# Kernel optimization log

Hardware: AMD Instinct MI355X
Metric: run time of the kernel (lower is better)

Reference implementation:

```python
import jax, jax.numpy as jnp
import numpy as np

N_NODES = 20000
IN_CH = 512
HEADS = 8
CH = 64  # hidden_layer per head
E = 320000
E_LABEL = 100000


def setup_inputs() -> dict:
    key = jax.random.key(0)
    ks = jax.random.split(key, 8)
    x = jax.random.normal(ks[0], (N_NODES, IN_CH), dtype=jnp.float32)
    edge_index = jax.random.randint(ks[1], (2, E), 0, N_NODES)
    edge_label_index = jax.random.randint(ks[2], (2, E_LABEL), 0, N_NODES)
    # GATv2Conv params (share_weights=False, bias=True)
    sc = 1.0 / np.sqrt(IN_CH)
    W_l = jax.random.normal(ks[3], (IN_CH, HEADS * CH), dtype=jnp.float32) * sc
    W_r = jax.random.normal(ks[4], (IN_CH, HEADS * CH), dtype=jnp.float32) * sc
    att = jax.random.normal(ks[5], (HEADS, CH), dtype=jnp.float32) * (1.0 / np.sqrt(CH))
    bias = jnp.zeros((HEADS * CH,), dtype=jnp.float32)
    gamma = jnp.ones((HEADS * CH,), dtype=jnp.float32)
    beta = jnp.zeros((HEADS * CH,), dtype=jnp.float32)
    return {"x": x, "edge_index": edge_index, "edge_label_index": edge_label_index,
            "W_l": W_l, "W_r": W_r, "att": att, "bias": bias,
            "gamma": gamma, "beta": beta}


def reference(x, edge_index, edge_label_index, W_l, W_r, att, bias, gamma, beta):
    N = x.shape[0]
    H, C = att.shape
    src, dst = edge_index[0], edge_index[1]
    # GATv2Conv: separate source/target linear maps
    xl = (x @ W_l).reshape(N, H, C)
    xr = (x @ W_r).reshape(N, H, C)
    # per-edge attention logits (GATv2: leaky_relu BEFORE attention vector)
    e = jax.nn.leaky_relu(xl[src] + xr[dst], negative_slope=0.2)  # [E,H,C]
    alpha = jnp.einsum('ehc,hc->eh', e, att)                      # [E,H]
    # softmax over incoming edges of each destination node
    amax = jax.ops.segment_max(alpha, dst, num_segments=N)        # [N,H]
    alpha = jnp.exp(alpha - amax[dst])
    denom = jax.ops.segment_sum(alpha, dst, num_segments=N)       # [N,H]
    alpha = alpha / (denom[dst] + 1e-16)
    # scatter-add aggregation of attended source messages
    out = jax.ops.segment_sum(alpha[:, :, None] * xl[src], dst, num_segments=N)  # [N,H,C]
    out = out.reshape(N, H * C) + bias
    # BatchNorm1d (training-mode batch stats, eps=1e-5)
    mu = out.mean(axis=0)
    var = out.var(axis=0)
    out = (out - mu) * jax.lax.rsqrt(var + 1e-5) * gamma + beta
    out = jax.nn.relu(out)  # dropout is identity in deterministic reference
    # gather + dot-product link scoring
    s = out[edge_label_index[0]]
    t = out[edge_label_index[1]]
    return jnp.sum(s * t, axis=1)  # [E_LABEL]
```

## Files before the change

kernel.cpp:

```cpp
#include <hip/hip_runtime.h>
#include <hip/hip_bf16.h>
#include <cstdint>

#define IN_CH 512
#define HC    512
#define HEADS 8
#define NPACK 1024

typedef __attribute__((ext_vector_type(8))) short bf16x8;
typedef __attribute__((ext_vector_type(8))) ushort u16x8;
typedef __attribute__((ext_vector_type(4))) float f32x4;
typedef const __attribute__((address_space(1))) uint8_t* gaddr_t;
typedef __attribute__((address_space(3))) uint8_t* laddr_t;

__device__ inline ushort f2bf(float f) {
  uint32_t u = __float_as_uint(f);
  return (ushort)((u + 0x7fffu + ((u >> 16) & 1u)) >> 16);
}
__device__ inline float bf2f(ushort u) {
  return __uint_as_float(((uint32_t)u) << 16);
}

__global__ void prep(const float* __restrict__ x, ushort* __restrict__ xb,
                     const float* __restrict__ Wl, const float* __restrict__ Wr,
                     ushort* __restrict__ bt,
                     const int* __restrict__ ei, int* __restrict__ counts,
                     const int* __restrict__ eli, int* __restrict__ counts2,
                     int n4, int E, int EL, int nbc, int nbp, int nbh) {
  const int b = blockIdx.x;
  if (b < nbc) {
    const int i = b * 256 + threadIdx.x;
    if (i < n4) {
      const float4 v = ((const float4*)x)[i];
      ushort4 o;
      o.x = f2bf(v.x); o.y = f2bf(v.y); o.z = f2bf(v.z); o.w = f2bf(v.w);
      ((ushort4*)xb)[i] = o;
    }
  } else if (b < nbc + nbp) {
    const int i = (b - nbc) * 256 + threadIdx.x;
    if (i < NPACK * IN_CH) {
      const int n = i >> 9, k = i & 511;
      const float v = (n < HC) ? Wl[(size_t)k * HC + n] : Wr[(size_t)k * HC + (n - HC)];
      bt[i] = f2bf(v);
    }
  } else if (b < nbc + nbp + nbh) {
    const int e = (b - nbc - nbp) * 256 + threadIdx.x;
    if (e < E) atomicAdd(&counts[ei[E + e]], 1);
  } else {
    const int e = (b - nbc - nbp - nbh) * 256 + threadIdx.x;
    if (e < EL) atomicAdd(&counts2[eli[e]], 1);
  }
}

__global__ __launch_bounds__(256) void gemm_mfma(
    const ushort* __restrict__ xb, const ushort* __restrict__ bt,
    ushort* __restrict__ xlb, float* __restrict__ xr, int M) {
  __shared__ __align__(16) ushort As[128 * 32];
  __shared__ __align__(16) ushort Bs[128 * 32];
  const int wave = threadIdx.x >> 6, lane = threadIdx.x & 63;
  const int row0 = blockIdx.y * 128, col0 = blockIdx.x * 128;
  const int quad = lane >> 4, m16 = lane & 15;
  const int wrow = (wave >> 1) * 64, wcol = (wave & 1) * 64;
  const int srow = lane >> 2;
  const int scol = (lane & 3) * 8;
  const f32x4 zero = {0.f, 0.f, 0.f, 0.f};
  f32x4 acc[4][4];
  #pragma unroll
  for (int i = 0; i < 4; ++i)
    #pragma unroll
    for (int j = 0; j < 4; ++j) acc[i][j] = zero;

  for (int k0 = 0; k0 < IN_CH; k0 += 32) {
    #pragma unroll
    for (int c = 0; c < 2; ++c) {
      const int chunk = wave * 2 + c;
      const ushort* ga = xb + (size_t)(row0 + chunk * 16 + srow) * IN_CH + k0 + scol;
      __builtin_amdgcn_global_load_lds((gaddr_t)ga, (laddr_t)(As + chunk * 512), 16, 0, 0);
      const ushort* gb = bt + (size_t)(col0 + chunk * 16 + srow) * IN_CH + k0 + scol;
      __builtin_amdgcn_global_load_lds((gaddr_t)gb, (laddr_t)(Bs + chunk * 512), 16, 0, 0);
    }
    __syncthreads();
    bf16x8 af[4], bfr[4];
    #pragma unroll
    for (int i = 0; i < 4; ++i)
      af[i] = *(const bf16x8*)(As + (wrow + i * 16 + m16) * 32 + quad * 8);
    #pragma unroll
    for (int j = 0; j < 4; ++j)
      bfr[j] = *(const bf16x8*)(Bs + (wcol + j * 16 + m16) * 32 + quad * 8);
    #pragma unroll
    for (int i = 0; i < 4; ++i)
      #pragma unroll
      for (int j = 0; j < 4; ++j)
        acc[i][j] = __builtin_amdgcn_mfma_f32_16x16x32_bf16(af[i], bfr[j], acc[i][j], 0, 0, 0);
    __syncthreads();
  }
  const bool isL = (col0 < HC);
  #pragma unroll
  for (int i = 0; i < 4; ++i) {
    const int r = row0 + wrow + i * 16 + quad * 4;
    #pragma unroll
    for (int j = 0; j < 4; ++j) {
      const int cg = col0 + wcol + j * 16 + m16;
      #pragma unroll
      for (int t = 0; t < 4; ++t) {
        const int rr = r + t;
        if (rr < M) {
          if (isL) xlb[(size_t)rr * HC + cg] = f2bf(acc[i][j][t]);
          else     xr[(size_t)rr * HC + (cg - HC)] = acc[i][j][t];
        }
      }
    }
  }
}

__global__ void scan1(const int* __restrict__ cA, int* __restrict__ oA, int* __restrict__ bA,
                      const int* __restrict__ cB, int* __restrict__ oB, int* __restrict__ bB,
                      int Nn, int nb) {
  const int half = (blockIdx.x >= nb) ? 1 : 0;
  const int blk  = blockIdx.x - half * nb;
  const int* counts = half ? cB : cA;
  int* offsets = half ? oB : oA;
  int* bsums   = half ? bB : bA;
  __shared__ int tmp[256];
  const int t = threadIdx.x;
  const int i = blk * 256 + t;
  const int v = (i < Nn) ? counts[i] : 0;
  tmp[t] = v;
  __syncthreads();
  for (int d = 1; d < 256; d <<= 1) {
    int add = (t >= d) ? tmp[t - d] : 0;
    __syncthreads();
    tmp[t] += add;
    __syncthreads();
  }
  if (i < Nn) offsets[i] = tmp[t] - v;
  if (t == 255) bsums[blk] = tmp[255];
}

__global__ void scan2(int* __restrict__ bA, int* __restrict__ bB, int nb) {
  int* bsums = blockIdx.x ? bB : bA;
  __shared__ int tmp[256];
  const int t = threadIdx.x;
  if (t < nb) tmp[t] = bsums[t];
  __syncthreads();
  if (t == 0) {
    int run = 0;
    for (int b = 0; b < nb; ++b) { int c = tmp[b]; tmp[b] = run; run += c; }
  }
  __syncthreads();
  if (t < nb) bsums[t] = tmp[t];
}

__global__ void scan3(int* __restrict__ oA, const int* __restrict__ bA, int* __restrict__ curA,
                      int* __restrict__ oB, const int* __restrict__ bB, int* __restrict__ curB,
                      int Nn, int nb) {
  const int half = (blockIdx.x >= nb) ? 1 : 0;
  const int blk  = blockIdx.x - half * nb;
  int* offsets = half ? oB : oA;
  const int* bsums = half ? bB : bA;
  int* cursor  = half ? curB : curA;
  const int i = blk * 256 + threadIdx.x;
  if (i < Nn) {
    const int o = offsets[i] + bsums[i >> 8];
    offsets[i] = o;
    cursor[i] = o;
  }
}

__global__ void csr_fill(const int* __restrict__ ei, int* __restrict__ cursor,
                         int* __restrict__ csr_src,
                         const int* __restrict__ eli, int* __restrict__ cursor2,
                         int* __restrict__ csr_t, int* __restrict__ csr_eid,
                         int E, int EL, int nbE) {
  const int b = blockIdx.x;
  if (b < nbE) {
    const int e = b * 256 + threadIdx.x;
    if (e < E) {
      const int pos = atomicAdd(&cursor[ei[E + e]], 1);
      csr_src[pos] = ei[e];
    }
  } else {
    const int e = (b - nbE) * 256 + threadIdx.x;
    if (e < EL) {
      const int pos = atomicAdd(&cursor2[eli[e]], 1);
      csr_t[pos] = eli[EL + e];
      csr_eid[pos] = e;
    }
  }
}

__global__ __launch_bounds__(256) void gatv2_agg(
    const ushort* __restrict__ xlb, const float* xr, const float* __restrict__ att,
    const int* __restrict__ offsets, const int* __restrict__ counts,
    const int* __restrict__ csr_src, float* agg, int Nn) {
  const int node = blockIdx.x * 4 + (threadIdx.x >> 6);
  const int lane = threadIdx.x & 63;
  if (node >= Nn) return;
  const int start = offsets[node];
  const int deg   = counts[node];
  float rv[8], tv[8];
  {
    const float4* pr = (const float4*)(xr + (size_t)node * HC + lane * 8);
    const float4 r0 = pr[0], r1 = pr[1];
    rv[0]=r0.x; rv[1]=r0.y; rv[2]=r0.z; rv[3]=r0.w;
    rv[4]=r1.x; rv[5]=r1.y; rv[6]=r1.z; rv[7]=r1.w;
    const float4* pa = (const float4*)(att + lane * 8);
    const float4 t0 = pa[0], t1 = pa[1];
    tv[0]=t0.x; tv[1]=t0.y; tv[2]=t0.z; tv[3]=t0.w;
    tv[4]=t1.x; tv[5]=t1.y; tv[6]=t1.z; tv[7]=t1.w;
  }
  float acc[8] = {};
  float densum = 0.f;
  const int* ps = csr_src + start;
  auto row = [&](int idx) {
    return *(const u16x8*)(xlb + (size_t)ps[idx] * HC + lane * 8);
  };
  auto body = [&](const u16x8 cur) {
    float a[8];
    #pragma unroll
    for (int c = 0; c < 8; ++c) a[c] = bf2f((ushort)cur[c]);
    float s = 0.f;
    #pragma unroll
    for (int c = 0; c < 8; ++c) {
      const float v = a[c] + rv[c];
      s += fmaxf(v, 0.2f * v) * tv[c];
    }
    s += __shfl_xor(s, 1, 8);
    s += __shfl_xor(s, 2, 8);
    s += __shfl_xor(s, 4, 8);
    const float ea = __expf(s);
    densum += ea;
    #pragma unroll
    for (int c = 0; c < 8; ++c) acc[c] += ea * a[c];
  };

  u16x8 v0 = {}, v1 = {};
  if (deg > 0) v0 = row(0);
  if (deg > 1) v1 = row(1);
  int i = 0;
  for (; i + 2 <= deg; i += 2) {
    const u16x8 c0 = v0;
    if (i + 2 < deg) v0 = row(i + 2);
    body(c0);
    const u16x8 c1 = v1;
    if (i + 3 < deg) v1 = row(i + 3);
    body(c1);
  }
  if (i < deg) body(v0);

  const float inv = 1.0f / (densum + 1e-16f);
  float* pd = agg + (size_t)node * HC + lane * 8;
  *(float4*)(pd + 0) = make_float4(acc[0] * inv, acc[1] * inv, acc[2] * inv, acc[3] * inv);
  *(float4*)(pd + 4) = make_float4(acc[4] * inv, acc[5] * inv, acc[6] * inv, acc[7] * inv);
}

__global__ void bn_stats(const float* __restrict__ agg, float* __restrict__ gsum,
                         float* __restrict__ gsq, int Nn) {
  const int t = threadIdx.x;
  const int rows_per_block = (Nn + gridDim.x - 1) / gridDim.x;
  const int r0 = blockIdx.x * rows_per_block;
  const int r1 = min(Nn, r0 + rows_per_block);
  float s0 = 0.f, s1 = 0.f, q0 = 0.f, q1 = 0.f;
  for (int r = r0; r < r1; ++r) {
    const float v0 = agg[(size_t)r * HC + t];
    const float v1 = agg[(size_t)r * HC + t + 256];
    s0 += v0; q0 += v0 * v0;
    s1 += v1; q1 += v1 * v1;
  }
  atomicAdd(&gsum[t], s0);
  atomicAdd(&gsum[t + 256], s1);
  atomicAdd(&gsq[t], q0);
  atomicAdd(&gsq[t + 256], q1);
}

__global__ void bn_final(const float* __restrict__ gsum, const float* __restrict__ gsq,
                         float* __restrict__ mu, float* __restrict__ rs, float invN) {
  const int c = threadIdx.x;
  const float m = gsum[c] * invN;
  const float v = gsq[c] * invN - m * m;
  mu[c] = m;
  rs[c] = rsqrtf(v + 1e-5f);
}

__global__ void bn_apply(const float* __restrict__ agg, const float* __restrict__ mu,
                         const float* __restrict__ rs, const float* __restrict__ gamma,
                         const float* __restrict__ beta, ushort* __restrict__ y, int total4) {
  const int i = blockIdx.x * blockDim.x + threadIdx.x;
  if (i >= total4) return;
  const int base = i << 2;
  const int c = base & (HC - 1);
  float4 v = *(const float4*)(agg + base);
  ushort4 o;
  o.x = f2bf(fmaxf(0.f, (v.x - mu[c + 0]) * rs[c + 0] * gamma[c + 0] + beta[c + 0]));
  o.y = f2bf(fmaxf(0.f, (v.y - mu[c + 1]) * rs[c + 1] * gamma[c + 1] + beta[c + 1]));
  o.z = f2bf(fmaxf(0.f, (v.z - mu[c + 2]) * rs[c + 2] * gamma[c + 2] + beta[c + 2]));
  o.w = f2bf(fmaxf(0.f, (v.w - mu[c + 3]) * rs[c + 3] * gamma[c + 3] + beta[c + 3]));
  *(ushort4*)(y + base) = o;
}

__global__ __launch_bounds__(256) void score_g(
    const ushort* __restrict__ y, const int* __restrict__ off2,
    const int* __restrict__ cnt2, const int* __restrict__ csr_t,
    const int* __restrict__ csr_eid, float* __restrict__ out, int Nn) {
  const int node = blockIdx.x * 4 + (threadIdx.x >> 6);
  const int lane = threadIdx.x & 63;
  if (node >= Nn) return;
  const int start = off2[node];
  const int deg   = cnt2[node];
  if (deg == 0) return;
  float a[8];
  {
    const u16x8 us = *(const u16x8*)(y + (size_t)node * HC + lane * 8);
    #pragma unroll
    for (int c = 0; c < 8; ++c) a[c] = bf2f((ushort)us[c]);
  }
  const int* pt = csr_t + start;
  const int* pe = csr_eid + start;
  auto row = [&](int idx) {
    return *(const u16x8*)(y + (size_t)pt[idx] * HC + lane * 8);
  };
  auto emit = [&](const u16x8 ut, int eid) {
    float s = 0.f;
    #pragma unroll
    for (int c = 0; c < 8; ++c) s += a[c] * bf2f((ushort)ut[c]);
    #pragma unroll
    for (int off = 32; off > 0; off >>= 1) s += __shfl_down(s, off, 64);
    if (lane == 0) out[eid] = s;
  };
  u16x8 v0 = {}, v1 = {};
  v0 = row(0);
  if (deg > 1) v1 = row(1);
  int j = 0;
  for (; j + 2 <= deg; j += 2) {
    const u16x8 c0 = v0;
    if (j + 2 < deg) v0 = row(j + 2);
    emit(c0, pe[j]);
    const u16x8 c1 = v1;
    if (j + 3 < deg) v1 = row(j + 3);
    emit(c1, pe[j + 1]);
  }
  if (j < deg) emit(v0, pe[j]);
}

extern "C" void kernel_launch(void* const* d_in, const int* in_sizes, int n_in,
                              void* d_out, int out_size, void* d_ws, size_t ws_size,
                              hipStream_t stream) {
  const float* x     = (const float*)d_in[0];
  const int*   ei    = (const int*)d_in[1];
  const int*   eli   = (const int*)d_in[2];
  const float* W_l   = (const float*)d_in[3];
  const float* W_r   = (const float*)d_in[4];
  const float* att   = (const float*)d_in[5];
  const float* gamma = (const float*)d_in[7];
  const float* beta  = (const float*)d_in[8];
  float* out = (float*)d_out;

  const int Nn = in_sizes[0] / IN_CH;
  const int E  = in_sizes[1] / 2;
  const int EL = in_sizes[2] / 2;

  ushort* xlb = (ushort*)d_ws;
  float*  xr  = (float*)(xlb + (size_t)Nn * HC);
  ushort* xbf = (ushort*)(xr + (size_t)Nn * HC);
  ushort* btb = xbf + (size_t)Nn * IN_CH;
  int* counts   = (int*)(btb + (size_t)NPACK * IN_CH);
  int* counts2  = counts + Nn;
  float* gsum   = (float*)(counts2 + Nn);
  float* gsq    = gsum + HC;
  int* offsets  = (int*)(gsq + HC);
  int* cursor   = offsets + Nn;
  int* bsumsA   = cursor + Nn;
  int* offsets2 = bsumsA + 256;
  int* cursor2  = offsets2 + Nn;
  int* bsumsB   = cursor2 + Nn;
  int* csr_src  = bsumsB + 256;
  int* csr_t    = csr_src + E;
  int* csr_eid  = csr_t + EL;
  float* mu     = (float*)(csr_eid + EL);
  float* rs     = mu + HC;
  float*  agg = xr;
  ushort* y   = xlb;

  const int nb  = (Nn + 255) / 256;
  const int nbc = (Nn * IN_CH / 4 + 255) / 256;
  const int nbp = (NPACK * IN_CH + 255) / 256;
  const int nbh = (E + 255) / 256;
  const int nbh2 = (EL + 255) / 256;

  hipMemsetAsync(counts, 0, (2 * (size_t)Nn + 2 * HC) * sizeof(int), stream);

  prep<<<nbc + nbp + nbh + nbh2, 256, 0, stream>>>(
      x, xbf, W_l, W_r, btb, ei, counts, eli, counts2,
      Nn * IN_CH / 4, E, EL, nbc, nbp, nbh);

  dim3 ggrid(NPACK / 128, (Nn + 127) / 128);
  gemm_mfma<<<ggrid, 256, 0, stream>>>(xbf, btb, xlb, xr, Nn);

  scan1<<<2 * nb, 256, 0, stream>>>(counts, offsets, bsumsA,
                                    counts2, offsets2, bsumsB, Nn, nb);
  scan2<<<2, 256, 0, stream>>>(bsumsA, bsumsB, nb);
  scan3<<<2 * nb, 256, 0, stream>>>(offsets, bsumsA, cursor,
                                    offsets2, bsumsB, cursor2, Nn, nb);
  csr_fill<<<nbh + nbh2, 256, 0, stream>>>(ei, cursor, csr_src,
                                           eli, cursor2, csr_t, csr_eid, E, EL, nbh);

  gatv2_agg<<<(Nn + 3) / 4, 256, 0, stream>>>(xlb, xr, att, offsets, counts,
                                              csr_src, agg, Nn);

  bn_stats<<<200, 256, 0, stream>>>(agg, gsum, gsq, Nn);
  bn_final<<<1, HC, 0, stream>>>(gsum, gsq, mu, rs, 1.0f / (float)Nn);
  bn_apply<<<(Nn * HC / 4 + 255) / 256, 256, 0, stream>>>(agg, mu, rs, gamma, beta, y,
                                                          Nn * HC / 4);

  score_g<<<(Nn + 3) / 4, 256, 0, stream>>>(y, offsets2, counts2, csr_t, csr_eid,
                                            out, Nn);
}
```

Before: 320.1 us.

## Store xr and aggregation in bf16, fold scan2 and bn_final, deepen prefetch

Stores the right-side projection and the aggregated output as bf16 instead of fp32, which halves their memory traffic in the GEMM epilogue, the aggregation, bn_stats and bn_apply. The separate scan2 and bn_final kernels are removed: scan3 computes each block prefix by reducing bsums itself, and bn_apply derives mean and rstd inline from the summed statistics. The gather loops in gatv2_agg and score_g now prefetch four rows instead of two. This cuts launch count and bandwidth at the cost of bf16 rounding on xr and on the pre-BatchNorm activations, plus some redundant per-thread work in bn_apply and scan3.

```diff
diff --git a/kernel.cpp b/kernel.cpp
--- a/kernel.cpp
+++ b/kernel.cpp
@@ -54,7 +54,7 @@
 
 __global__ __launch_bounds__(256) void gemm_mfma(
     const ushort* __restrict__ xb, const ushort* __restrict__ bt,
-    ushort* __restrict__ xlb, float* __restrict__ xr, int M) {
+    ushort* __restrict__ xlb, ushort* __restrict__ xrb, int M) {
   __shared__ __align__(16) ushort As[128 * 32];
   __shared__ __align__(16) ushort Bs[128 * 32];
   const int wave = threadIdx.x >> 6, lane = threadIdx.x & 63;
@@ -95,19 +95,18 @@
     __syncthreads();
   }
   const bool isL = (col0 < HC);
+  ushort* dst = isL ? xlb : xrb;
+  const int cbase = isL ? col0 : (col0 - HC);
   #pragma unroll
   for (int i = 0; i < 4; ++i) {
     const int r = row0 + wrow + i * 16 + quad * 4;
     #pragma unroll
     for (int j = 0; j < 4; ++j) {
-      const int cg = col0 + wcol + j * 16 + m16;
+      const int cg = cbase + wcol + j * 16 + m16;
       #pragma unroll
       for (int t = 0; t < 4; ++t) {
         const int rr = r + t;
-        if (rr < M) {
-          if (isL) xlb[(size_t)rr * HC + cg] = f2bf(acc[i][j][t]);
-          else     xr[(size_t)rr * HC + (cg - HC)] = acc[i][j][t];
-        }
+        if (rr < M) dst[(size_t)rr * HC + cg] = f2bf(acc[i][j][t]);
       }
     }
   }
@@ -137,20 +136,6 @@
   if (t == 255) bsums[blk] = tmp[255];
 }
 
-__global__ void scan2(int* __restrict__ bA, int* __restrict__ bB, int nb) {
-  int* bsums = blockIdx.x ? bB : bA;
-  __shared__ int tmp[256];
-  const int t = threadIdx.x;
-  if (t < nb) tmp[t] = bsums[t];
-  __syncthreads();
-  if (t == 0) {
-    int run = 0;
-    for (int b = 0; b < nb; ++b) { int c = tmp[b]; tmp[b] = run; run += c; }
-  }
-  __syncthreads();
-  if (t < nb) bsums[t] = tmp[t];
-}
-
 __global__ void scan3(int* __restrict__ oA, const int* __restrict__ bA, int* __restrict__ curA,
                       int* __restrict__ oB, const int* __restrict__ bB, int* __restrict__ curB,
                       int Nn, int nb) {
@@ -159,9 +144,18 @@
   int* offsets = half ? oB : oA;
   const int* bsums = half ? bB : bA;
   int* cursor  = half ? curB : curA;
+  __shared__ int pref;
+  if (threadIdx.x < 64) {
+    int s = 0;
+    for (int b = threadIdx.x; b < blk; b += 64) s += bsums[b];
+    #pragma unroll
+    for (int off = 32; off > 0; off >>= 1) s += __shfl_down(s, off, 64);
+    if (threadIdx.x == 0) pref = s;
+  }
+  __syncthreads();
   const int i = blk * 256 + threadIdx.x;
   if (i < Nn) {
-    const int o = offsets[i] + bsums[i >> 8];
+    const int o = offsets[i] + pref;
     offsets[i] = o;
     cursor[i] = o;
   }
@@ -190,9 +184,9 @@
 }
 
 __global__ __launch_bounds__(256) void gatv2_agg(
-    const ushort* __restrict__ xlb, const float* xr, const float* __restrict__ att,
+    const ushort* __restrict__ xlb, const ushort* xrb, const float* __restrict__ att,
     const int* __restrict__ offsets, const int* __restrict__ counts,
-    const int* __restrict__ csr_src, float* agg, int Nn) {
+    const int* __restrict__ csr_src, ushort* agg, int Nn) {
   const int node = blockIdx.x * 4 + (threadIdx.x >> 6);
   const int lane = threadIdx.x & 63;
   if (node >= Nn) return;
@@ -200,10 +194,9 @@
   const int deg   = counts[node];
   float rv[8], tv[8];
   {
-    const float4* pr = (const float4*)(xr + (size_t)node * HC + lane * 8);
-    const float4 r0 = pr[0], r1 = pr[1];
-    rv[0]=r0.x; rv[1]=r0.y; rv[2]=r0.z; rv[3]=r0.w;
-    rv[4]=r1.x; rv[5]=r1.y; rv[6]=r1.z; rv[7]=r1.w;
+    const u16x8 ur = *(const u16x8*)(xrb + (size_t)node * HC + lane * 8);
+    #pragma unroll
+    for (int c = 0; c < 8; ++c) rv[c] = bf2f((ushort)ur[c]);
     const float4* pa = (const float4*)(att + lane * 8);
     const float4 t0 = pa[0], t1 = pa[1];
     tv[0]=t0.x; tv[1]=t0.y; tv[2]=t0.z; tv[3]=t0.w;
@@ -234,27 +227,36 @@
     for (int c = 0; c < 8; ++c) acc[c] += ea * a[c];
   };
 
-  u16x8 v0 = {}, v1 = {};
-  if (deg > 0) v0 = row(0);
-  if (deg > 1) v1 = row(1);
+  u16x8 b0 = {}, b1 = {}, b2 = {}, b3 = {};
+  if (deg > 0) b0 = row(0);
+  if (deg > 1) b1 = row(1);
+  if (deg > 2) b2 = row(2);
+  if (deg > 3) b3 = row(3);
   int i = 0;
-  for (; i + 2 <= deg; i += 2) {
-    const u16x8 c0 = v0;
-    if (i + 2 < deg) v0 = row(i + 2);
-    body(c0);
-    const u16x8 c1 = v1;
-    if (i + 3 < deg) v1 = row(i + 3);
-    body(c1);
-  }
-  if (i < deg) body(v0);
+  for (; i + 4 <= deg; i += 4) {
+    const u16x8 c0 = b0; if (i + 4 < deg) b0 = row(i + 4);
+    const u16x8 c1 = b1; if (i + 5 < deg) b1 = row(i + 5);
+    const u16x8 c2 = b2; if (i + 6 < deg) b2 = row(i + 6);
+    const u16x8 c3 = b3; if (i + 7 < deg) b3 = row(i + 7);
+    body(c0); body(c1); body(c2); body(c3);
+  }
+  const int r = deg - i;
+  if (r > 0) body(b0);
+  if (r > 1) body(b1);
+  if (r > 2) body(b2);
 
   const float inv = 1.0f / (densum + 1e-16f);
-  float* pd = agg + (size_t)node * HC + lane * 8;
-  *(float4*)(pd + 0) = make_float4(acc[0] * inv, acc[1] * inv, acc[2] * inv, acc[3] * inv);
-  *(float4*)(pd + 4) = make_float4(acc[4] * inv, acc[5] * inv, acc[6] * inv, acc[7] * inv);
-}
-
-__global__ void bn_stats(const float* __restrict__ agg, float* __restrict__ gsum,
+  ushort* pd = agg + (size_t)node * HC + lane * 8;
+  ushort4 o0, o1;
+  o0.x = f2bf(acc[0] * inv); o0.y = f2bf(acc[1] * inv);
+  o0.z = f2bf(acc[2] * inv); o0.w = f2bf(acc[3] * inv);
+  o1.x = f2bf(acc[4] * inv); o1.y = f2bf(acc[5] * inv);
+  o1.z = f2bf(acc[6] * inv); o1.w = f2bf(acc[7] * inv);
+  *(ushort4*)(pd + 0) = o0;
+  *(ushort4*)(pd + 4) = o1;
+}
+
+__global__ void bn_stats(const ushort* __restrict__ agg, float* __restrict__ gsum,
                          float* __restrict__ gsq, int Nn) {
   const int t = threadIdx.x;
   const int rows_per_block = (Nn + gridDim.x - 1) / gridDim.x;
@@ -262,39 +264,40 @@
   const int r1 = min(Nn, r0 + rows_per_block);
   float s0 = 0.f, s1 = 0.f, q0 = 0.f, q1 = 0.f;
   for (int r = r0; r < r1; ++r) {
-    const float v0 = agg[(size_t)r * HC + t];
-    const float v1 = agg[(size_t)r * HC + t + 256];
+    const ushort2 u = ((const ushort2*)(agg + (size_t)r * HC))[t];
+    const float v0 = bf2f(u.x), v1 = bf2f(u.y);
     s0 += v0; q0 += v0 * v0;
     s1 += v1; q1 += v1 * v1;
   }
-  atomicAdd(&gsum[t], s0);
-  atomicAdd(&gsum[t + 256], s1);
-  atomicAdd(&gsq[t], q0);
-  atomicAdd(&gsq[t + 256], q1);
-}
-
-__global__ void bn_final(const float* __restrict__ gsum, const float* __restrict__ gsq,
-                         float* __restrict__ mu, float* __restrict__ rs, float invN) {
-  const int c = threadIdx.x;
-  const float m = gsum[c] * invN;
-  const float v = gsq[c] * invN - m * m;
-  mu[c] = m;
-  rs[c] = rsqrtf(v + 1e-5f);
-}
-
-__global__ void bn_apply(const float* __restrict__ agg, const float* __restrict__ mu,
-                         const float* __restrict__ rs, const float* __restrict__ gamma,
-                         const float* __restrict__ beta, ushort* __restrict__ y, int total4) {
+  atomicAdd(&gsum[2 * t], s0);
+  atomicAdd(&gsum[2 * t + 1], s1);
+  atomicAdd(&gsq[2 * t], q0);
+  atomicAdd(&gsq[2 * t + 1], q1);
+}
+
+__global__ void bn_apply(const ushort* __restrict__ agg, const float* __restrict__ gsum,
+                         const float* __restrict__ gsq, const float* __restrict__ gamma,
+                         const float* __restrict__ beta, ushort* __restrict__ y,
+                         float invN, int total4) {
   const int i = blockIdx.x * blockDim.x + threadIdx.x;
   if (i >= total4) return;
   const int base = i << 2;
   const int c = base & (HC - 1);
-  float4 v = *(const float4*)(agg + base);
+  const float4 gs = *(const float4*)(gsum + c);
+  const float4 gq = *(const float4*)(gsq + c);
+  const float4 ga = *(const float4*)(gamma + c);
+  const float4 be = *(const float4*)(beta + c);
+  const ushort4 u = *(const ushort4*)(agg + base);
+  float m, var;
   ushort4 o;
-  o.x = f2bf(fmaxf(0.f, (v.x - mu[c + 0]) * rs[c + 0] * gamma[c + 0] + beta[c + 0]));
-  o.y = f2bf(fmaxf(0.f, (v.y - mu[c + 1]) * rs[c + 1] * gamma[c + 1] + beta[c + 1]));
-  o.z = f2bf(fmaxf(0.f, (v.z - mu[c + 2]) * rs[c + 2] * gamma[c + 2] + beta[c + 2]));
-  o.w = f2bf(fmaxf(0.f, (v.w - mu[c + 3]) * rs[c + 3] * gamma[c + 3] + beta[c + 3]));
+  m = gs.x * invN; var = gq.x * invN - m * m;
+  o.x = f2bf(fmaxf(0.f, (bf2f(u.x) - m) * rsqrtf(var + 1e-5f) * ga.x + be.x));
+  m = gs.y * invN; var = gq.y * invN - m * m;
+  o.y = f2bf(fmaxf(0.f, (bf2f(u.y) - m) * rsqrtf(var + 1e-5f) * ga.y + be.y));
+  m = gs.z * invN; var = gq.z * invN - m * m;
+  o.z = f2bf(fmaxf(0.f, (bf2f(u.z) - m) * rsqrtf(var + 1e-5f) * ga.z + be.z));
+  m = gs.w * invN; var = gq.w * invN - m * m;
+  o.w = f2bf(fmaxf(0.f, (bf2f(u.w) - m) * rsqrtf(var + 1e-5f) * ga.w + be.w));
   *(ushort4*)(y + base) = o;
 }
 
@@ -327,19 +330,23 @@
     for (int off = 32; off > 0; off >>= 1) s += __shfl_down(s, off, 64);
     if (lane == 0) out[eid] = s;
   };
-  u16x8 v0 = {}, v1 = {};
-  v0 = row(0);
-  if (deg > 1) v1 = row(1);
+  u16x8 b0 = {}, b1 = {}, b2 = {}, b3 = {};
+  b0 = row(0);
+  if (deg > 1) b1 = row(1);
+  if (deg > 2) b2 = row(2);
+  if (deg > 3) b3 = row(3);
   int j = 0;
-  for (; j + 2 <= deg; j += 2) {
-    const u16x8 c0 = v0;
-    if (j + 2 < deg) v0 = row(j + 2);
-    emit(c0, pe[j]);
-    const u16x8 c1 = v1;
-    if (j + 3 < deg) v1 = row(j + 3);
-    emit(c1, pe[j + 1]);
-  }
-  if (j < deg) emit(v0, pe[j]);
+  for (; j + 4 <= deg; j += 4) {
+    const u16x8 c0 = b0; if (j + 4 < deg) b0 = row(j + 4);
+    const u16x8 c1 = b1; if (j + 5 < deg) b1 = row(j + 5);
+    const u16x8 c2 = b2; if (j + 6 < deg) b2 = row(j + 6);
+    const u16x8 c3 = b3; if (j + 7 < deg) b3 = row(j + 7);
+    emit(c0, pe[j]); emit(c1, pe[j + 1]); emit(c2, pe[j + 2]); emit(c3, pe[j + 3]);
+  }
+  const int r = deg - j;
+  if (r > 0) emit(b0, pe[j]);
+  if (r > 1) emit(b1, pe[j + 1]);
+  if (r > 2) emit(b2, pe[j + 2]);
 }
 
 extern "C" void kernel_launch(void* const* d_in, const int* in_sizes, int n_in,
@@ -360,8 +367,8 @@
   const int EL = in_sizes[2] / 2;
 
   ushort* xlb = (ushort*)d_ws;
-  float*  xr  = (float*)(xlb + (size_t)Nn * HC);
-  ushort* xbf = (ushort*)(xr + (size_t)Nn * HC);
+  ushort* xrb = xlb + (size_t)Nn * HC;
+  ushort* xbf = xrb + (size_t)Nn * HC;
   ushort* btb = xbf + (size_t)Nn * IN_CH;
   int* counts   = (int*)(btb + (size_t)NPACK * IN_CH);
   int* counts2  = counts + Nn;
@@ -376,9 +383,7 @@
   int* csr_src  = bsumsB + 256;
   int* csr_t    = csr_src + E;
   int* csr_eid  = csr_t + EL;
-  float* mu     = (float*)(csr_eid + EL);
-  float* rs     = mu + HC;
-  float*  agg = xr;
+  ushort* agg = xrb;
   ushort* y   = xlb;
 
   const int nb  = (Nn + 255) / 256;
@@ -394,23 +399,21 @@
       Nn * IN_CH / 4, E, EL, nbc, nbp, nbh);
 
   dim3 ggrid(NPACK / 128, (Nn + 127) / 128);
-  gemm_mfma<<<ggrid, 256, 0, stream>>>(xbf, btb, xlb, xr, Nn);
+  gemm_mfma<<<ggrid, 256, 0, stream>>>(xbf, btb, xlb, xrb, Nn);
 
   scan1<<<2 * nb, 256, 0, stream>>>(counts, offsets, bsumsA,
                                     counts2, offsets2, bsumsB, Nn, nb);
-  scan2<<<2, 256, 0, stream>>>(bsumsA, bsumsB, nb);
   scan3<<<2 * nb, 256, 0, stream>>>(offsets, bsumsA, cursor,
                                     offsets2, bsumsB, cursor2, Nn, nb);
   csr_fill<<<nbh + nbh2, 256, 0, stream>>>(ei, cursor, csr_src,
                                            eli, cursor2, csr_t, csr_eid, E, EL, nbh);
 
-  gatv2_agg<<<(Nn + 3) / 4, 256, 0, stream>>>(xlb, xr, att, offsets, counts,
+  gatv2_agg<<<(Nn + 3) / 4, 256, 0, stream>>>(xlb, xrb, att, offsets, counts,
                                               csr_src, agg, Nn);
 
   bn_stats<<<200, 256, 0, stream>>>(agg, gsum, gsq, Nn);
-  bn_final<<<1, HC, 0, stream>>>(gsum, gsq, mu, rs, 1.0f / (float)Nn);
-  bn_apply<<<(Nn * HC / 4 + 255) / 256, 256, 0, stream>>>(agg, mu, rs, gamma, beta, y,
-                                                          Nn * HC / 4);
+  bn_apply<<<(Nn * HC / 4 + 255) / 256, 256, 0, stream>>>(
+      agg, gsum, gsq, gamma, beta, y, 1.0f / (float)Nn, Nn * HC / 4);
 
   score_g<<<(Nn + 3) / 4, 256, 0, stream>>>(y, offsets2, counts2, csr_t, csr_eid,
                                             out, Nn);
```

Result: no change. 318.6 us (-0.5%).
